# Performance work log

Hardware: AMD Instinct MI355X
Metric: run time of the kernel (lower is better)

The kernel has to match this reference:

```python
import jax, jax.numpy as jnp
import numpy as np

NEG_INF = -9e16
SLOPE = 0.2  # leaky relu slope


def setup_inputs() -> dict:
    key = jax.random.key(0)
    k1, k2, k3, k4 = jax.random.split(key, 4)
    N, F_in, H, D = 3072, 512, 8, 64
    h = jax.random.normal(k1, (N, F_in), dtype=jnp.float32)
    adj = jax.random.randint(k2, (N, N), 0, 2, dtype=jnp.int32)
    W = jax.random.normal(k3, (H, F_in, D), dtype=jnp.float32) * (2.0 / (F_in + D)) ** 0.5
    a = jax.random.normal(k4, (H, 2 * D, 1), dtype=jnp.float32) * (2.0 / (2 * D + 1)) ** 0.5
    return {"h": h, "adj": adj, "W": W, "a": a}


def reference(h, adj, W, a):
    # h: [N, F], W: [H, F, D], a: [H, 2D, 1], adj: [N, N]
    H, _, D = W.shape
    ht = jnp.einsum("nf,hfd->hnd", h, W)            # [H, N, D]
    a_src = a[:, :D, 0]                               # [H, D]
    a_dst = a[:, D:, 0]                               # [H, D]
    src = jnp.einsum("hnd,hd->hn", ht, a_src)        # [H, N]
    dst = jnp.einsum("hnd,hd->hn", ht, a_dst)        # [H, N]
    e = src[:, :, None] + dst[:, None, :]             # [H, N, N]
    e = jnp.where(e > 0, e, SLOPE * e)                # leaky relu
    e = jnp.where(adj[None] > 0, e, NEG_INF)
    att = jax.nn.softmax(e, axis=-1)                  # [H, N, N]
    hp = jnp.einsum("hnm,hmd->hnd", att, ht)         # [H, N, D]
    out = jnp.transpose(hp, (1, 0, 2)).reshape(h.shape[0], H * D)  # concat heads
    return (out, att)
```

## Files before the change

kernel.cpp:

```cpp
#include <hip/hip_runtime.h>

#define NN 3072
#define FF 512
#define HH 8
#define DD 64
#define SLOPEV 0.2f
#define CH 128
#define NC (NN/CH)

typedef __bf16  bf16x8 __attribute__((ext_vector_type(8)));
typedef __bf16  bf16x4 __attribute__((ext_vector_type(4)));
typedef short   s16x8  __attribute__((ext_vector_type(8)));
typedef float   f32x4  __attribute__((ext_vector_type(4)));
typedef unsigned long long u64;

#define MFMA16(a,b,c) __builtin_amdgcn_mfma_f32_16x16x32_bf16((a),(b),(c),0,0,0)

__device__ __forceinline__ short f2bf(float x){ __bf16 b=(__bf16)x; return __builtin_bit_cast(short,b); }
__device__ __forceinline__ float bf2f(short s){ return (float)__builtin_bit_cast(__bf16,s); }
__device__ __forceinline__ bf16x8 ldbf8(const short* p){ return __builtin_bit_cast(bf16x8, *(const s16x8*)p); }

__device__ __forceinline__ void gload16(const void* g, void* l){
  __builtin_amdgcn_global_load_lds(
      (const __attribute__((address_space(1))) void*)(uintptr_t)g,
      (__attribute__((address_space(3))) void*)(uint32_t)(uintptr_t)l, 16, 0, 0);
}

__global__ __launch_bounds__(256) void k_prep1(const float* __restrict__ W,
    const int* __restrict__ adj,
    short* __restrict__ wthi, short* __restrict__ wtlo, u64* __restrict__ padj){
  int bid = blockIdx.x, t = threadIdx.x;
  if (bid < 128){
    int uid = bid*4 + (t>>6);
    int h = uid>>6, f0 = (uid&63)*8, d = t&63;
    s16x8 vh, vl;
    #pragma unroll
    for (int j=0;j<8;j++){
      float v = W[((size_t)h*FF + f0 + j)*DD + d];
      short s = f2bf(v); vh[j]=s; vl[j]=f2bf(v-bf2f(s));
    }
    size_t o = ((size_t)h*DD + d)*FF + f0;
    *(s16x8*)(wthi+o)=vh; *(s16x8*)(wtlo+o)=vl;
  } else {
    const int total = NN*NN;
    for (int idx = (bid-128)*256 + t; idx < total; idx += 1024*256){
      u64 b = __ballot(adj[idx] > 0);
      if ((t & 63) == 0) padj[idx>>6] = b;
    }
  }
}

__global__ __launch_bounds__(256) void k_prep2(const float* __restrict__ h,
    const short* __restrict__ wthi, const short* __restrict__ wtlo,
    const float* __restrict__ a,
    float* __restrict__ src, float* __restrict__ dst, short* __restrict__ hthi){
  __shared__ short tH[2][64][40];
  int bid = blockIdx.x, t = threadIdx.x;
  int uu = t>>7, tid = t&127;
  int unit = bid*2 + uu;
  int hh = unit/96, n0 = (unit%96)*32;
  int w = tid>>6, lane = tid&63;
  int r15 = lane&15, g = lane>>4;
  int arow = n0 + w*16 + r15;
  f32x4 acc[4] = {{0.f,0.f,0.f,0.f},{0.f,0.f,0.f,0.f},{0.f,0.f,0.f,0.f},{0.f,0.f,0.f,0.f}};
  const float* ha = h + (size_t)arow*FF + g*8;
  for (int kk=0; kk<FF; kk+=32){
    float4 x0 = *(const float4*)(ha+kk), x1 = *(const float4*)(ha+kk+4);
    float xv[8] = {x0.x,x0.y,x0.z,x0.w,x1.x,x1.y,x1.z,x1.w};
    bf16x8 ahi, alo;
    #pragma unroll
    for (int e=0;e<8;e++){
      short s = f2bf(xv[e]);
      ahi[e] = __builtin_bit_cast(__bf16, s);
      alo[e] = (__bf16)(xv[e] - bf2f(s));
    }
    #pragma unroll
    for (int c=0;c<4;c++){
      size_t bo = ((size_t)hh*DD + c*16 + r15)*FF + g*8 + kk;
      bf16x8 bh = ldbf8(wthi + bo), bl = ldbf8(wtlo + bo);
      acc[c] = MFMA16(ahi,bh,acc[c]);
      acc[c] = MFMA16(ahi,bl,acc[c]);
      acc[c] = MFMA16(alo,bh,acc[c]);
    }
  }

  float asv[4], adv[4];
  #pragma unroll
  for (int c=0;c<4;c++){
    asv[c] = a[hh*2*DD + c*16 + r15];
    adv[c] = a[hh*2*DD + DD + c*16 + r15];
  }
  #pragma unroll
  for (int r=0;r<4;r++){
    float ps = acc[0][r]*asv[0] + acc[1][r]*asv[1] + acc[2][r]*asv[2] + acc[3][r]*asv[3];
    float pd = acc[0][r]*adv[0] + acc[1][r]*adv[1] + acc[2][r]*adv[2] + acc[3][r]*adv[3];
    #pragma unroll
    for (int m=1;m<16;m<<=1){ ps += __shfl_xor(ps,m,64); pd += __shfl_xor(pd,m,64); }
    if (r15 == 0){
      int n = n0 + w*16 + g*4 + r;
      src[hh*NN + n] = ps;
      dst[hh*NN + n] = pd;
    }
  }

  #pragma unroll
  for (int c=0;c<4;c++){
    #pragma unroll
    for (int r=0;r<4;r++){
      int dloc = c*16 + r15, nloc = w*16 + g*4 + r;
      tH[uu][dloc][nloc] = f2bf(acc[c][r]);
    }
  }
  __syncthreads();
  int row = tid>>1, half = tid&1;
  size_t o = ((size_t)hh*DD + row)*NN + n0 + half*16;
  *(s16x8*)(hthi + o)     = *(const s16x8*)&tH[uu][row][half*16];
  *(s16x8*)(hthi + o + 8) = *(const s16x8*)&tH[uu][row][half*16+8];
}

__global__ __launch_bounds__(512, 6) void k_att(const u64* __restrict__ padj,
    const float* __restrict__ src, const float* __restrict__ dst,
    const short* __restrict__ hthi, float* __restrict__ dout){
  __shared__ short hA[64][CH], hB[64][CH];
  __shared__ short pA[32][CH], pB[32][CH];
  const size_t OUTOFF = (size_t)NN*HH*DD;
  int bid = blockIdx.x;
  int h = bid & 7, n0 = (bid >> 3) * 32;
  int t = threadIdx.x;
  int r = t>>4, j = t&15;
  int nrow = n0 + r;
  float srcv = src[h*NN + nrow];
  const float* dsth = dst + h*NN;
  const u64* arow = padj + (size_t)nrow*(NN/64);

  int wv = t>>6, lane = t&63, r15 = lane&15, g = lane>>4;
  int cblk = wv&3, nh = wv>>2;
  int drow = t>>4;
  int sslot = (t&15) ^ (drow&7);
  const short* ghA = hthi + ((size_t)(h*DD) + drow)*NN + sslot*8;
  const short* ghB = hthi + ((size_t)(h*DD) + drow + 32)*NN + sslot*8;

  gload16(ghA, &hA[wv*4][0]);
  gload16(ghB, &hA[32 + wv*4][0]);
  __builtin_amdgcn_sched_barrier(0);

  float psum = 0.f;
  for (int c=0;c<NC;c++){
    u64 w0 = arow[c*2], w1 = arow[c*2+1];
    const float* dp = dsth + c*CH + j*4;
    float4 d0 = *(const float4*)dp, d1 = *(const float4*)(dp+64);
    float dj[8] = {d0.x,d0.y,d0.z,d0.w,d1.x,d1.y,d1.z,d1.w};
    #pragma unroll
    for (int e=0;e<8;e++){
      float ev = srcv + dj[e];
      ev = fmaxf(ev, SLOPEV*ev);
      u64 bits = (e<4) ? w0 : w1;
      float p = ((bits >> (j*4 + (e&3))) & 1ull) ? __expf(ev) : 0.f;
      psum += p;
    }
  }
  #pragma unroll
  for (int m=1;m<16;m<<=1) psum += __shfl_xor(psum, m, 64);
  float inv = (psum > 0.f) ? 1.f/psum : (1.f/(float)NN);
  bool am = !(psum > 0.f);

  f32x4 acc = {0.f,0.f,0.f,0.f};
  float* attrow = dout + OUTOFF + ((size_t)(h*NN + nrow))*NN;
  int aoff0 = (cblk*16 + r15)*(CH*2);
  int boff0 = (nh*16 + r15)*(CH*2);
  int csw   = (r15&7)<<4;
  int xw    = (r&7)<<4;
  int pof0  = r*(CH*2) + ((j*8) ^ xw);
  int pof1  = r*(CH*2) + ((128 + j*8) ^ xw);
  const float* dvp = dsth + j*4;

  u64 w0 = arow[0], w1 = arow[1];
  float4 dva = *(const float4*)dvp;
  float4 dvb = *(const float4*)(dvp + 64);

  for (int c=0;c<NC;c++){
    short (*hc)[CH] = (c&1)?hB:hA;
    short (*hn)[CH] = (c&1)?hA:hB;
    short (*pc)[CH] = (c&1)?pB:pA;

    int cn = (c+1 < NC) ? c+1 : NC-1;
    u64 w0n = arow[cn*2], w1n = arow[cn*2+1];
    float4 dva_n = *(const float4*)(dvp + cn*CH);
    float4 dvb_n = *(const float4*)(dvp + cn*CH + 64);

    float o[8];
    #pragma unroll
    for (int e=0;e<4;e++){
      float ev = srcv + ((const float*)&dva)[e];
      ev = fmaxf(ev, SLOPEV*ev);
      float p = ((w0 >> (j*4 + e)) & 1ull) ? __expf(ev) : 0.f;
      if (am) p = 1.f;
      o[e] = p * inv;
      float ev2 = srcv + ((const float*)&dvb)[e];
      ev2 = fmaxf(ev2, SLOPEV*ev2);
      float p2 = ((w1 >> (j*4 + e)) & 1ull) ? __expf(ev2) : 0.f;
      if (am) p2 = 1.f;
      o[4+e] = p2 * inv;
    }
    f32x4 s0 = {o[0],o[1],o[2],o[3]};
    f32x4 s1 = {o[4],o[5],o[6],o[7]};
    __builtin_nontemporal_store(s0, (f32x4*)(attrow + c*CH + j*4));
    __builtin_nontemporal_store(s1, (f32x4*)(attrow + c*CH + 64 + j*4));
    bf16x4 p0, p1;
    #pragma unroll
    for (int e=0;e<4;e++){ p0[e] = (__bf16)o[e]; p1[e] = (__bf16)o[4+e]; }
    *(bf16x4*)((char*)pc + pof0) = p0;
    *(bf16x4*)((char*)pc + pof1) = p1;

    __builtin_amdgcn_sched_barrier(0);
    asm volatile("s_waitcnt vmcnt(5) lgkmcnt(0)" ::: "memory");
    __builtin_amdgcn_sched_barrier(0);
    __builtin_amdgcn_s_barrier();
    __builtin_amdgcn_sched_barrier(0);

    const char* hcB = (const char*)hc;
    const char* pcB = (const char*)pc;
    #pragma unroll
    for (int ks=0;ks<4;ks++){
      int kb = (ks*64 + g*16) ^ csw;
      bf16x8 bf = *(const bf16x8*)(pcB + boff0 + kb);
      bf16x8 ah = *(const bf16x8*)(hcB + aoff0 + kb);
      acc = MFMA16(ah, bf, acc);
    }

    if (c+1 < NC){
      gload16(ghA + (c+1)*CH, &hn[wv*4][0]);
      gload16(ghB + (c+1)*CH, &hn[32 + wv*4][0]);
    }
    __builtin_amdgcn_sched_barrier(0);

    w0 = w0n; w1 = w1n; dva = dva_n; dvb = dvb_n;
  }

  int n = n0 + nh*16 + r15;
  size_t ob = (size_t)n*(HH*DD) + h*DD + cblk*16 + g*4;
  __builtin_nontemporal_store(acc, (f32x4*)(dout+ob));
}

extern "C" void kernel_launch(void* const* d_in, const int* in_sizes, int n_in,
                              void* d_out, int out_size, void* d_ws, size_t ws_size,
                              hipStream_t stream) {
  const float* h   = (const float*)d_in[0];
  const int*   adj = (const int*)d_in[1];
  const float* W   = (const float*)d_in[2];
  const float* a   = (const float*)d_in[3];
  float* out = (float*)d_out;

  short* wthi = (short*)d_ws;
  short* wtlo = wthi + (size_t)HH*DD*FF;
  short* hthi = wtlo + (size_t)HH*DD*FF;
  float* srcb = (float*)(hthi + (size_t)HH*DD*NN);
  float* dstb = srcb + HH*NN;
  u64*   padj = (u64*)(dstb + HH*NN);

  k_prep1<<<dim3(1152), 256, 0, stream>>>(W, adj, wthi, wtlo, padj);
  k_prep2<<<dim3(384), 256, 0, stream>>>(h, wthi, wtlo, a, srcb, dstb, hthi);
  k_att  <<<dim3(NN/32*HH), 512, 0, stream>>>(padj, srcb, dstb, hthi, out);
}
```

Before: 136.6 us.

## Load MFMA A operands from global into registers instead of LDS staging

Drops the LDS double buffers for the transposed features. Each lane now loads its own MFMA A-fragments (four bf16x8 vectors) straight from global memory into registers, prefetching the next chunk one iteration ahead. The vmcnt wait before the barrier is removed and LDS use falls to the probability tiles only, which may help occupancy. In exchange, lanes with the same row across the two nh-halves load duplicate data, global loads are less coalesced (16-byte strided rows), and register pressure rises.

```diff
diff --git a/kernel.cpp b/kernel.cpp
--- a/kernel.cpp
+++ b/kernel.cpp
@@ -19,12 +19,6 @@
 __device__ __forceinline__ short f2bf(float x){ __bf16 b=(__bf16)x; return __builtin_bit_cast(short,b); }
 __device__ __forceinline__ float bf2f(short s){ return (float)__builtin_bit_cast(__bf16,s); }
 __device__ __forceinline__ bf16x8 ldbf8(const short* p){ return __builtin_bit_cast(bf16x8, *(const s16x8*)p); }
-
-__device__ __forceinline__ void gload16(const void* g, void* l){
-  __builtin_amdgcn_global_load_lds(
-      (const __attribute__((address_space(1))) void*)(uintptr_t)g,
-      (__attribute__((address_space(3))) void*)(uint32_t)(uintptr_t)l, 16, 0, 0);
-}
 
 __global__ __launch_bounds__(256) void k_prep1(const float* __restrict__ W,
     const int* __restrict__ adj,
@@ -121,7 +115,6 @@
 __global__ __launch_bounds__(512, 6) void k_att(const u64* __restrict__ padj,
     const float* __restrict__ src, const float* __restrict__ dst,
     const short* __restrict__ hthi, float* __restrict__ dout){
-  __shared__ short hA[64][CH], hB[64][CH];
   __shared__ short pA[32][CH], pB[32][CH];
   const size_t OUTOFF = (size_t)NN*HH*DD;
   int bid = blockIdx.x;
@@ -135,14 +128,7 @@
 
   int wv = t>>6, lane = t&63, r15 = lane&15, g = lane>>4;
   int cblk = wv&3, nh = wv>>2;
-  int drow = t>>4;
-  int sslot = (t&15) ^ (drow&7);
-  const short* ghA = hthi + ((size_t)(h*DD) + drow)*NN + sslot*8;
-  const short* ghB = hthi + ((size_t)(h*DD) + drow + 32)*NN + sslot*8;
-
-  gload16(ghA, &hA[wv*4][0]);
-  gload16(ghB, &hA[32 + wv*4][0]);
-  __builtin_amdgcn_sched_barrier(0);
+  const short* gah = hthi + ((size_t)(h*DD) + cblk*16 + r15)*NN + g*8;
 
   float psum = 0.f;
   for (int c=0;c<NC;c++){
@@ -166,7 +152,6 @@
 
   f32x4 acc = {0.f,0.f,0.f,0.f};
   float* attrow = dout + OUTOFF + ((size_t)(h*NN + nrow))*NN;
-  int aoff0 = (cblk*16 + r15)*(CH*2);
   int boff0 = (nh*16 + r15)*(CH*2);
   int csw   = (r15&7)<<4;
   int xw    = (r&7)<<4;
@@ -177,16 +162,23 @@
   u64 w0 = arow[0], w1 = arow[1];
   float4 dva = *(const float4*)dvp;
   float4 dvb = *(const float4*)(dvp + 64);
+  bf16x8 ac0 = ldbf8(gah);
+  bf16x8 ac1 = ldbf8(gah + 32);
+  bf16x8 ac2 = ldbf8(gah + 64);
+  bf16x8 ac3 = ldbf8(gah + 96);
 
   for (int c=0;c<NC;c++){
-    short (*hc)[CH] = (c&1)?hB:hA;
-    short (*hn)[CH] = (c&1)?hA:hB;
     short (*pc)[CH] = (c&1)?pB:pA;
 
     int cn = (c+1 < NC) ? c+1 : NC-1;
     u64 w0n = arow[cn*2], w1n = arow[cn*2+1];
     float4 dva_n = *(const float4*)(dvp + cn*CH);
     float4 dvb_n = *(const float4*)(dvp + cn*CH + 64);
+    const short* gan = gah + cn*CH;
+    bf16x8 an0 = ldbf8(gan);
+    bf16x8 an1 = ldbf8(gan + 32);
+    bf16x8 an2 = ldbf8(gan + 64);
+    bf16x8 an3 = ldbf8(gan + 96);
 
     float o[8];
     #pragma unroll
@@ -213,27 +205,24 @@
     *(bf16x4*)((char*)pc + pof1) = p1;
 
     __builtin_amdgcn_sched_barrier(0);
-    asm volatile("s_waitcnt vmcnt(5) lgkmcnt(0)" ::: "memory");
+    asm volatile("s_waitcnt lgkmcnt(0)" ::: "memory");
     __builtin_amdgcn_sched_barrier(0);
     __builtin_amdgcn_s_barrier();
     __builtin_amdgcn_sched_barrier(0);
 
-    const char* hcB = (const char*)hc;
     const char* pcB = (const char*)pc;
-    #pragma unroll
-    for (int ks=0;ks<4;ks++){
-      int kb = (ks*64 + g*16) ^ csw;
-      bf16x8 bf = *(const bf16x8*)(pcB + boff0 + kb);
-      bf16x8 ah = *(const bf16x8*)(hcB + aoff0 + kb);
-      acc = MFMA16(ah, bf, acc);
-    }
-
-    if (c+1 < NC){
-      gload16(ghA + (c+1)*CH, &hn[wv*4][0]);
-      gload16(ghB + (c+1)*CH, &hn[32 + wv*4][0]);
-    }
-    __builtin_amdgcn_sched_barrier(0);
-
+    {
+      bf16x8 bf0 = *(const bf16x8*)(pcB + boff0 + ((0*64 + g*16) ^ csw));
+      acc = MFMA16(ac0, bf0, acc);
+      bf16x8 bf1 = *(const bf16x8*)(pcB + boff0 + ((1*64 + g*16) ^ csw));
+      acc = MFMA16(ac1, bf1, acc);
+      bf16x8 bf2 = *(const bf16x8*)(pcB + boff0 + ((2*64 + g*16) ^ csw));
+      acc = MFMA16(ac2, bf2, acc);
+      bf16x8 bf3 = *(const bf16x8*)(pcB + boff0 + ((3*64 + g*16) ^ csw));
+      acc = MFMA16(ac3, bf3, acc);
+    }
+
+    ac0 = an0; ac1 = an1; ac2 = an2; ac3 = an3;
     w0 = w0n; w1 = w1n; dva = dva_n; dvb = dvb_n;
   }
 
```

Result: slower. 161.3 us (+18.1%).

## Fuse projection, adjacency packing and attention into one kernel with grid barrier

Applied to the files above, without the earlier changes.

Merges the projection GEMM (src/dst/hthi) and the adjacency bit-packing into the attention kernel. The first two waves of each block compute the projection tile while the remaining six waves pack their slice of adj. All blocks then meet at a global atomic barrier before the attention phase starts. This removes one kernel launch and its inter-kernel gap, and overlaps packing with the GEMM. It depends on all 768 blocks being co-resident, otherwise the barrier deadlocks, and it adds a memset for the barrier counter.

```diff
diff --git a/kernel.cpp b/kernel.cpp
--- a/kernel.cpp
+++ b/kernel.cpp
@@ -7,12 +7,14 @@
 #define SLOPEV 0.2f
 #define CH 128
 #define NC (NN/CH)
+#define NBLK (NN/32*HH)
 
 typedef __bf16  bf16x8 __attribute__((ext_vector_type(8)));
 typedef __bf16  bf16x4 __attribute__((ext_vector_type(4)));
 typedef short   s16x8  __attribute__((ext_vector_type(8)));
 typedef float   f32x4  __attribute__((ext_vector_type(4)));
 typedef unsigned long long u64;
+typedef unsigned int u32;
 
 #define MFMA16(a,b,c) __builtin_amdgcn_mfma_f32_16x16x32_bf16((a),(b),(c),0,0,0)
 
@@ -26,119 +28,125 @@
       (__attribute__((address_space(3))) void*)(uint32_t)(uintptr_t)l, 16, 0, 0);
 }
 
-__global__ __launch_bounds__(256) void k_prep1(const float* __restrict__ W,
-    const int* __restrict__ adj,
-    short* __restrict__ wthi, short* __restrict__ wtlo, u64* __restrict__ padj){
+__global__ __launch_bounds__(256) void k_wt(const float* __restrict__ W,
+    short* __restrict__ wthi, short* __restrict__ wtlo){
   int bid = blockIdx.x, t = threadIdx.x;
-  if (bid < 128){
-    int uid = bid*4 + (t>>6);
-    int h = uid>>6, f0 = (uid&63)*8, d = t&63;
-    s16x8 vh, vl;
-    #pragma unroll
-    for (int j=0;j<8;j++){
-      float v = W[((size_t)h*FF + f0 + j)*DD + d];
-      short s = f2bf(v); vh[j]=s; vl[j]=f2bf(v-bf2f(s));
-    }
-    size_t o = ((size_t)h*DD + d)*FF + f0;
-    *(s16x8*)(wthi+o)=vh; *(s16x8*)(wtlo+o)=vl;
-  } else {
-    const int total = NN*NN;
-    for (int idx = (bid-128)*256 + t; idx < total; idx += 1024*256){
-      u64 b = __ballot(adj[idx] > 0);
-      if ((t & 63) == 0) padj[idx>>6] = b;
-    }
-  }
-}
-
-__global__ __launch_bounds__(256) void k_prep2(const float* __restrict__ h,
+  int uid = bid*4 + (t>>6);
+  int h = uid>>6, f0 = (uid&63)*8, d = t&63;
+  s16x8 vh, vl;
+  #pragma unroll
+  for (int j=0;j<8;j++){
+    float v = W[((size_t)h*FF + f0 + j)*DD + d];
+    short s = f2bf(v); vh[j]=s; vl[j]=f2bf(v-bf2f(s));
+  }
+  size_t o = ((size_t)h*DD + d)*FF + f0;
+  *(s16x8*)(wthi+o)=vh; *(s16x8*)(wtlo+o)=vl;
+}
+
+__global__ __launch_bounds__(512, 6) void k_fused(const float* __restrict__ hx,
     const short* __restrict__ wthi, const short* __restrict__ wtlo,
-    const float* __restrict__ a,
-    float* __restrict__ src, float* __restrict__ dst, short* __restrict__ hthi){
-  __shared__ short tH[2][64][40];
-  int bid = blockIdx.x, t = threadIdx.x;
-  int uu = t>>7, tid = t&127;
-  int unit = bid*2 + uu;
-  int hh = unit/96, n0 = (unit%96)*32;
-  int w = tid>>6, lane = tid&63;
-  int r15 = lane&15, g = lane>>4;
-  int arow = n0 + w*16 + r15;
-  f32x4 acc[4] = {{0.f,0.f,0.f,0.f},{0.f,0.f,0.f,0.f},{0.f,0.f,0.f,0.f},{0.f,0.f,0.f,0.f}};
-  const float* ha = h + (size_t)arow*FF + g*8;
-  for (int kk=0; kk<FF; kk+=32){
-    float4 x0 = *(const float4*)(ha+kk), x1 = *(const float4*)(ha+kk+4);
-    float xv[8] = {x0.x,x0.y,x0.z,x0.w,x1.x,x1.y,x1.z,x1.w};
-    bf16x8 ahi, alo;
-    #pragma unroll
-    for (int e=0;e<8;e++){
-      short s = f2bf(xv[e]);
-      ahi[e] = __builtin_bit_cast(__bf16, s);
-      alo[e] = (__bf16)(xv[e] - bf2f(s));
-    }
-    #pragma unroll
-    for (int c=0;c<4;c++){
-      size_t bo = ((size_t)hh*DD + c*16 + r15)*FF + g*8 + kk;
-      bf16x8 bh = ldbf8(wthi + bo), bl = ldbf8(wtlo + bo);
-      acc[c] = MFMA16(ahi,bh,acc[c]);
-      acc[c] = MFMA16(ahi,bl,acc[c]);
-      acc[c] = MFMA16(alo,bh,acc[c]);
-    }
-  }
-
-  float asv[4], adv[4];
-  #pragma unroll
-  for (int c=0;c<4;c++){
-    asv[c] = a[hh*2*DD + c*16 + r15];
-    adv[c] = a[hh*2*DD + DD + c*16 + r15];
-  }
-  #pragma unroll
-  for (int r=0;r<4;r++){
-    float ps = acc[0][r]*asv[0] + acc[1][r]*asv[1] + acc[2][r]*asv[2] + acc[3][r]*asv[3];
-    float pd = acc[0][r]*adv[0] + acc[1][r]*adv[1] + acc[2][r]*adv[2] + acc[3][r]*adv[3];
-    #pragma unroll
-    for (int m=1;m<16;m<<=1){ ps += __shfl_xor(ps,m,64); pd += __shfl_xor(pd,m,64); }
-    if (r15 == 0){
-      int n = n0 + w*16 + g*4 + r;
-      src[hh*NN + n] = ps;
-      dst[hh*NN + n] = pd;
-    }
-  }
-
-  #pragma unroll
-  for (int c=0;c<4;c++){
-    #pragma unroll
-    for (int r=0;r<4;r++){
-      int dloc = c*16 + r15, nloc = w*16 + g*4 + r;
-      tH[uu][dloc][nloc] = f2bf(acc[c][r]);
-    }
-  }
-  __syncthreads();
-  int row = tid>>1, half = tid&1;
-  size_t o = ((size_t)hh*DD + row)*NN + n0 + half*16;
-  *(s16x8*)(hthi + o)     = *(const s16x8*)&tH[uu][row][half*16];
-  *(s16x8*)(hthi + o + 8) = *(const s16x8*)&tH[uu][row][half*16+8];
-}
-
-__global__ __launch_bounds__(512, 6) void k_att(const u64* __restrict__ padj,
-    const float* __restrict__ src, const float* __restrict__ dst,
-    const short* __restrict__ hthi, float* __restrict__ dout){
+    const float* __restrict__ av, const int* __restrict__ adj,
+    u64* __restrict__ padj, float* __restrict__ srcb, float* __restrict__ dstb,
+    short* __restrict__ hthi, u32* __restrict__ bar, float* __restrict__ dout){
   __shared__ short hA[64][CH], hB[64][CH];
   __shared__ short pA[32][CH], pB[32][CH];
   const size_t OUTOFF = (size_t)NN*HH*DD;
   int bid = blockIdx.x;
-  int h = bid & 7, n0 = (bid >> 3) * 32;
+  int h8 = bid & 7, n0 = (bid >> 3) * 32;
   int t = threadIdx.x;
+
+  short* tH = &pA[0][0];
+  if (t < 128){
+    int tid = t;
+    int w = tid>>6, lane = tid&63;
+    int r15 = lane&15, g = lane>>4;
+    int arow = n0 + w*16 + r15;
+    f32x4 acc4[4] = {{0.f,0.f,0.f,0.f},{0.f,0.f,0.f,0.f},{0.f,0.f,0.f,0.f},{0.f,0.f,0.f,0.f}};
+    const float* ha = hx + (size_t)arow*FF + g*8;
+    for (int kk=0; kk<FF; kk+=32){
+      float4 x0 = *(const float4*)(ha+kk), x1 = *(const float4*)(ha+kk+4);
+      float xv[8] = {x0.x,x0.y,x0.z,x0.w,x1.x,x1.y,x1.z,x1.w};
+      bf16x8 ahi, alo;
+      #pragma unroll
+      for (int e=0;e<8;e++){
+        short s = f2bf(xv[e]);
+        ahi[e] = __builtin_bit_cast(__bf16, s);
+        alo[e] = (__bf16)(xv[e] - bf2f(s));
+      }
+      #pragma unroll
+      for (int c=0;c<4;c++){
+        size_t bo = ((size_t)h8*DD + c*16 + r15)*FF + g*8 + kk;
+        bf16x8 bh = ldbf8(wthi + bo), bl = ldbf8(wtlo + bo);
+        acc4[c] = MFMA16(ahi,bh,acc4[c]);
+        acc4[c] = MFMA16(ahi,bl,acc4[c]);
+        acc4[c] = MFMA16(alo,bh,acc4[c]);
+      }
+    }
+    float asv[4], adv[4];
+    #pragma unroll
+    for (int c=0;c<4;c++){
+      asv[c] = av[h8*2*DD + c*16 + r15];
+      adv[c] = av[h8*2*DD + DD + c*16 + r15];
+    }
+    #pragma unroll
+    for (int r=0;r<4;r++){
+      float ps = acc4[0][r]*asv[0] + acc4[1][r]*asv[1] + acc4[2][r]*asv[2] + acc4[3][r]*asv[3];
+      float pd = acc4[0][r]*adv[0] + acc4[1][r]*adv[1] + acc4[2][r]*adv[2] + acc4[3][r]*adv[3];
+      #pragma unroll
+      for (int m=1;m<16;m<<=1){ ps += __shfl_xor(ps,m,64); pd += __shfl_xor(pd,m,64); }
+      if (r15 == 0){
+        int n = n0 + w*16 + g*4 + r;
+        srcb[h8*NN + n] = ps;
+        dstb[h8*NN + n] = pd;
+      }
+    }
+    #pragma unroll
+    for (int c=0;c<4;c++){
+      #pragma unroll
+      for (int r=0;r<4;r++){
+        int dloc = c*16 + r15, nloc = w*16 + g*4 + r;
+        tH[dloc*40 + nloc] = f2bf(acc4[c][r]);
+      }
+    }
+  } else {
+    int wv2 = (t>>6) - 2, lane = t&63;
+    int base = bid*12288 + wv2*2048;
+    #pragma unroll 4
+    for (int it=0; it<32; it++){
+      int idx = base + it*64 + lane;
+      u64 b = __ballot(adj[idx] > 0);
+      if (lane == 0) padj[idx>>6] = b;
+    }
+  }
+  __syncthreads();
+  if (t < 128){
+    int row = t>>1, half = t&1;
+    size_t o = ((size_t)h8*DD + row)*NN + n0 + half*16;
+    *(s16x8*)(hthi + o)     = *(const s16x8*)&tH[row*40 + half*16];
+    *(s16x8*)(hthi + o + 8) = *(const s16x8*)&tH[row*40 + half*16 + 8];
+  }
+
+  __syncthreads();
+  __threadfence();
+  if (t == 0){
+    __hip_atomic_fetch_add(bar, 1u, __ATOMIC_ACQ_REL, __HIP_MEMORY_SCOPE_AGENT);
+    while (__hip_atomic_load(bar, __ATOMIC_ACQUIRE, __HIP_MEMORY_SCOPE_AGENT) < (u32)NBLK)
+      __builtin_amdgcn_s_sleep(2);
+  }
+  __syncthreads();
+
   int r = t>>4, j = t&15;
   int nrow = n0 + r;
-  float srcv = src[h*NN + nrow];
-  const float* dsth = dst + h*NN;
+  float srcv = srcb[h8*NN + nrow];
+  const float* dsth = dstb + h8*NN;
   const u64* arow = padj + (size_t)nrow*(NN/64);
 
   int wv = t>>6, lane = t&63, r15 = lane&15, g = lane>>4;
   int cblk = wv&3, nh = wv>>2;
   int drow = t>>4;
   int sslot = (t&15) ^ (drow&7);
-  const short* ghA = hthi + ((size_t)(h*DD) + drow)*NN + sslot*8;
-  const short* ghB = hthi + ((size_t)(h*DD) + drow + 32)*NN + sslot*8;
+  const short* ghA = hthi + ((size_t)(h8*DD) + drow)*NN + sslot*8;
+  const short* ghB = hthi + ((size_t)(h8*DD) + drow + 32)*NN + sslot*8;
 
   gload16(ghA, &hA[wv*4][0]);
   gload16(ghB, &hA[32 + wv*4][0]);
@@ -165,7 +173,7 @@
   bool am = !(psum > 0.f);
 
   f32x4 acc = {0.f,0.f,0.f,0.f};
-  float* attrow = dout + OUTOFF + ((size_t)(h*NN + nrow))*NN;
+  float* attrow = dout + OUTOFF + ((size_t)(h8*NN + nrow))*NN;
   int aoff0 = (cblk*16 + r15)*(CH*2);
   int boff0 = (nh*16 + r15)*(CH*2);
   int csw   = (r15&7)<<4;
@@ -238,7 +246,7 @@
   }
 
   int n = n0 + nh*16 + r15;
-  size_t ob = (size_t)n*(HH*DD) + h*DD + cblk*16 + g*4;
+  size_t ob = (size_t)n*(HH*DD) + h8*DD + cblk*16 + g*4;
   __builtin_nontemporal_store(acc, (f32x4*)(dout+ob));
 }
 
@@ -257,8 +265,10 @@
   float* srcb = (float*)(hthi + (size_t)HH*DD*NN);
   float* dstb = srcb + HH*NN;
   u64*   padj = (u64*)(dstb + HH*NN);
-
-  k_prep1<<<dim3(1152), 256, 0, stream>>>(W, adj, wthi, wtlo, padj);
-  k_prep2<<<dim3(384), 256, 0, stream>>>(h, wthi, wtlo, a, srcb, dstb, hthi);
-  k_att  <<<dim3(NN/32*HH), 512, 0, stream>>>(padj, srcb, dstb, hthi, out);
-}
+  u32*   bar  = (u32*)(padj + (size_t)NN*NN/64);
+
+  hipMemsetAsync(bar, 0, sizeof(u32), stream);
+  k_wt<<<dim3(128), 256, 0, stream>>>(W, wthi, wtlo);
+  k_fused<<<dim3(NBLK), 512, 0, stream>>>(h, wthi, wtlo, a, adj,
+                                          padj, srcb, dstb, hthi, bar, out);
+}
```

Result: slower. 253.0 us (+85.3%).
